# Kernel tuning notes

Measured on AMD Instinct MI355X. Metric: run time of the kernel, lower is better.

## Reference

```python
import jax, jax.numpy as jnp
import numpy as np

B, L, D = 8, 512, 1024
NUM_SPANS = 6144  # L * max_width


def setup_inputs() -> dict:
    key = jax.random.key(0)
    k_h, k_s, k_w, k_b = jax.random.split(key, 4)
    h = jax.random.normal(k_h, (B, L, D), dtype=jnp.float32)
    span_idx = jax.random.randint(k_s, (B, NUM_SPANS, 2), 0, L, dtype=jnp.int64)
    # Linear(hidden, hidden) params (xavier-ish scale)
    lim = float(np.sqrt(6.0 / (D + D)))
    W = jax.random.uniform(k_w, (D, D), dtype=jnp.float32, minval=-lim, maxval=lim)
    b = jnp.zeros((D,), dtype=jnp.float32)
    return {"h": h, "span_idx": span_idx, "W": W, "b": b}


def reference(h, span_idx, W, b):
    # h: [B, L, D]; span_idx: [B, S, 2] with S = L * width
    Bb, Ll, Dd = h.shape
    start = jnp.clip(span_idx[..., 0], 0, Ll - 1)  # [B, S]
    end = jnp.clip(span_idx[..., 1], 0, Ll - 1)    # [B, S]
    valid = start <= end                            # [B, S]
    # prefix sums: cs[i, t] = sum_{u < t} h[i, u]  -> [B, L+1, D]
    cs = jnp.concatenate([jnp.zeros((Bb, 1, Dd), h.dtype), jnp.cumsum(h, axis=1)], axis=1)
    span_sum = (jnp.take_along_axis(cs, (end + 1)[:, :, None], axis=1)
                - jnp.take_along_axis(cs, start[:, :, None], axis=1))  # [B, S, D]
    count = (end - start + 1).astype(h.dtype)[:, :, None]
    span_rep = jnp.where(valid[:, :, None], span_sum / count, 0.0)  # [B, S, D]
    out = jax.nn.relu(jnp.einsum('bsd,ed->bse', span_rep, W) + b)
    return out.reshape(Bb, Ll, -1, Dd)
```

## Files before the change

### kernel.cpp

```cpp
#include <hip/hip_runtime.h>
#include <stdint.h>

#define B_DIM 8
#define L_DIM 512
#define D_DIM 1024
#define S_DIM 6144
#define M_DIM (B_DIM * S_DIM)
#define NCHUNK 8
#define CHUNK (L_DIM / NCHUNK)

typedef __attribute__((ext_vector_type(8))) short short8;
typedef __attribute__((ext_vector_type(4))) float f32x4;
typedef __attribute__((ext_vector_type(8))) unsigned short us8;

__device__ __forceinline__ unsigned short f2bf(float f) {
    unsigned int u = __float_as_uint(f);
    u += 0x7FFFu + ((u >> 16) & 1u);
    return (unsigned short)(u >> 16);
}

__global__ __launch_bounds__(256) void chunk_sums(const float* __restrict__ h,
                                                  float* __restrict__ csum) {
    int tid = blockIdx.x * 256 + threadIdx.x;
    int d = tid & 1023;
    int c = (tid >> 10) & 7;
    int b = tid >> 13;
    const float* hp = h + ((size_t)b * L_DIM + c * CHUNK) * D_DIM + d;
    float s = 0.f;
    #pragma unroll 8
    for (int i = 0; i < CHUNK; ++i) s += hp[(size_t)i * D_DIM];
    csum[tid] = s;
}

__global__ __launch_bounds__(256) void build_cs(const float* __restrict__ h,
                                                const float* __restrict__ csum,
                                                float* __restrict__ cs) {
    int tid = blockIdx.x * 256 + threadIdx.x;
    int d = tid & 1023;
    int c = (tid >> 10) & 7;
    int b = tid >> 13;
    float p = 0.f;
    for (int cc = 0; cc < c; ++cc)
        p += csum[(b << 13) + (cc << 10) + d];
    const float* hp = h + ((size_t)b * L_DIM + c * CHUNK) * D_DIM + d;
    float* cp = cs + ((size_t)b * (L_DIM + 1) + c * CHUNK) * D_DIM + d;
    if (c == 0) cp[0] = 0.f;
    #pragma unroll 8
    for (int i = 0; i < CHUNK; ++i) {
        p += hp[(size_t)i * D_DIM];
        cp[(size_t)(i + 1) * D_DIM] = p;
    }
}

__global__ __launch_bounds__(256) void spanrep(const float* __restrict__ cs,
                                               const int* __restrict__ span_idx,
                                               unsigned short* __restrict__ rep) {
    int tid = blockIdx.x * 256 + threadIdx.x;
    int d8 = tid & 127;
    int bs = tid >> 7;
    int b = bs / S_DIM;
    int2 se = ((const int2*)span_idx)[bs];
    int st = min(max(se.x, 0), L_DIM - 1);
    int en = min(max(se.y, 0), L_DIM - 1);
    bool valid = st <= en;
    float inv = valid ? 1.0f / (float)(en - st + 1) : 0.0f;
    const float* base = cs + (size_t)b * (L_DIM + 1) * D_DIM + d8 * 8;
    const float4* pe = (const float4*)(base + (size_t)(en + 1) * D_DIM);
    const float4* ps = (const float4*)(base + (size_t)st * D_DIM);
    float4 e0 = pe[0], e1 = pe[1];
    float4 s0 = ps[0], s1 = ps[1];
    us8 o;
    o[0] = f2bf((e0.x - s0.x) * inv);
    o[1] = f2bf((e0.y - s0.y) * inv);
    o[2] = f2bf((e0.z - s0.z) * inv);
    o[3] = f2bf((e0.w - s0.w) * inv);
    o[4] = f2bf((e1.x - s1.x) * inv);
    o[5] = f2bf((e1.y - s1.y) * inv);
    o[6] = f2bf((e1.z - s1.z) * inv);
    o[7] = f2bf((e1.w - s1.w) * inv);
    *(us8*)&rep[(size_t)bs * D_DIM + d8 * 8] = o;
}

__global__ __launch_bounds__(256) void wconv(const float* __restrict__ W,
                                             unsigned short* __restrict__ Wbf) {
    int tid = blockIdx.x * 256 + threadIdx.x;
    const float4* p = (const float4*)(W + (size_t)tid * 8);
    float4 a = p[0], c = p[1];
    us8 o;
    o[0] = f2bf(a.x); o[1] = f2bf(a.y); o[2] = f2bf(a.z); o[3] = f2bf(a.w);
    o[4] = f2bf(c.x); o[5] = f2bf(c.y); o[6] = f2bf(c.z); o[7] = f2bf(c.w);
    *(us8*)&Wbf[(size_t)tid * 8] = o;
}

__global__ __launch_bounds__(256) void gemm_bias_relu(
    const unsigned short* __restrict__ A,
    const unsigned short* __restrict__ Wt,
    const float* __restrict__ bias,
    float* __restrict__ out) {
    constexpr int K = D_DIM, N = D_DIM;
    __shared__ __align__(16) unsigned short As[128 * 64];
    __shared__ __align__(16) unsigned short Bs[128 * 64];
    const int tid = threadIdx.x;
    const int wid = tid >> 6, lane = tid & 63;
    const int bn = blockIdx.x & 7;
    const int bm = blockIdx.x >> 3;
    const int wr = wid >> 1, wc = wid & 1;
    const int rowA = bm * 128;
    const int rowB = bn * 128;

    f32x4 acc[4][4];
    #pragma unroll
    for (int i = 0; i < 4; ++i)
        #pragma unroll
        for (int j = 0; j < 4; ++j) acc[i][j] = (f32x4){0.f, 0.f, 0.f, 0.f};

    for (int k0 = 0; k0 < K; k0 += 64) {
        #pragma unroll
        for (int inst = 0; inst < 4; ++inst) {
            int e = inst * 2048 + tid * 8;
            int r = e >> 6, c = e & 63;
            const unsigned short* srcA = A + (size_t)(rowA + r) * K + (k0 + c);
            const unsigned short* srcB = Wt + (size_t)(rowB + r) * K + (k0 + c);
            __builtin_amdgcn_global_load_lds(
                (const __attribute__((address_space(1))) void*)srcA,
                (__attribute__((address_space(3))) void*)&As[inst * 2048 + wid * 512],
                16, 0, 0);
            __builtin_amdgcn_global_load_lds(
                (const __attribute__((address_space(1))) void*)srcB,
                (__attribute__((address_space(3))) void*)&Bs[inst * 2048 + wid * 512],
                16, 0, 0);
        }
        asm volatile("s_waitcnt vmcnt(0)" ::: "memory");
        __syncthreads();

        #pragma unroll
        for (int ks = 0; ks < 2; ++ks) {
            const int kc = ks * 32 + (lane >> 4) * 8;
            short8 af[4], bf[4];
            #pragma unroll
            for (int i = 0; i < 4; ++i) {
                af[i] = *(const short8*)&As[(wr * 64 + i * 16 + (lane & 15)) * 64 + kc];
                bf[i] = *(const short8*)&Bs[(wc * 64 + i * 16 + (lane & 15)) * 64 + kc];
            }
            #pragma unroll
            for (int i = 0; i < 4; ++i)
                #pragma unroll
                for (int j = 0; j < 4; ++j)
                    acc[i][j] = __builtin_amdgcn_mfma_f32_16x16x32_bf16(
                        af[i], bf[j], acc[i][j], 0, 0, 0);
        }
        __syncthreads();
    }

    const int m0 = rowA + wr * 64;
    const int n0 = rowB + wc * 64;
    const int rq = lane >> 4;
    const int cl = lane & 15;
    float bv[4];
    #pragma unroll
    for (int j = 0; j < 4; ++j) bv[j] = bias[n0 + j * 16 + cl];
    #pragma unroll
    for (int i = 0; i < 4; ++i)
        #pragma unroll
        for (int j = 0; j < 4; ++j)
            #pragma unroll
            for (int r = 0; r < 4; ++r) {
                int m = m0 + i * 16 + rq * 4 + r;
                int n = n0 + j * 16 + cl;
                float v = acc[i][j][r] + bv[j];
                out[(size_t)m * N + n] = v > 0.f ? v : 0.f;
            }
}

extern "C" void kernel_launch(void* const* d_in, const int* in_sizes, int n_in,
                              void* d_out, int out_size, void* d_ws, size_t ws_size,
                              hipStream_t stream) {
    const float* h = (const float*)d_in[0];
    const int* span = (const int*)d_in[1];
    const float* W = (const float*)d_in[2];
    const float* bias = (const float*)d_in[3];
    float* out = (float*)d_out;

    char* ws = (char*)d_ws;
    float* cs = (float*)(ws);
    unsigned short* Wbf = (unsigned short*)(ws + 16809984);
    float* csum = (float*)(ws + 18907136);
    unsigned short* rep = (unsigned short*)(ws + 19169280);

    chunk_sums<<<256, 256, 0, stream>>>(h, csum);
    build_cs<<<256, 256, 0, stream>>>(h, csum, cs);
    wconv<<<512, 256, 0, stream>>>(W, Wbf);
    spanrep<<<24576, 256, 0, stream>>>(cs, span, rep);
    gemm_bias_relu<<<3072, 256, 0, stream>>>(rep, Wbf, bias, out);
}
```

Baseline: 409.1 us.

## Fuse span-mean gather into GEMM with double-buffered swizzled LDS tiles

Removes the separate spanrep kernel and its bf16 intermediate. The GEMM now gathers prefix-sum rows directly, computes span means and writes them into swizzled LDS. The GEMM moves to 512-thread blocks with 128x256 tiles, double-buffered LDS for A and B, an XOR swizzle against bank conflicts, and a block-index swizzle for L2 locality. Each N-tile re-gathers the cs rows (4x redundant reads of fp32 cs), and register pressure rises with the prefetched float4s.

```diff
diff --git a/kernel.cpp b/kernel.cpp
--- a/kernel.cpp
+++ b/kernel.cpp
@@ -1,17 +1,23 @@
 #include <hip/hip_runtime.h>
+#include <hip/hip_bf16.h>
 #include <stdint.h>
 
 #define B_DIM 8
 #define L_DIM 512
 #define D_DIM 1024
 #define S_DIM 6144
-#define M_DIM (B_DIM * S_DIM)
 #define NCHUNK 8
 #define CHUNK (L_DIM / NCHUNK)
+#define CSB (513 * 1024)
 
 typedef __attribute__((ext_vector_type(8))) short short8;
 typedef __attribute__((ext_vector_type(4))) float f32x4;
 typedef __attribute__((ext_vector_type(8))) unsigned short us8;
+
+__device__ __forceinline__ unsigned short bf16b(float x) {
+    __hip_bfloat16 h = __float2bfloat16(x);
+    return *reinterpret_cast<unsigned short*>(&h);
+}
 
 __device__ __forceinline__ unsigned short f2bf(float f) {
     unsigned int u = __float_as_uint(f);
@@ -52,35 +58,6 @@
     }
 }
 
-__global__ __launch_bounds__(256) void spanrep(const float* __restrict__ cs,
-                                               const int* __restrict__ span_idx,
-                                               unsigned short* __restrict__ rep) {
-    int tid = blockIdx.x * 256 + threadIdx.x;
-    int d8 = tid & 127;
-    int bs = tid >> 7;
-    int b = bs / S_DIM;
-    int2 se = ((const int2*)span_idx)[bs];
-    int st = min(max(se.x, 0), L_DIM - 1);
-    int en = min(max(se.y, 0), L_DIM - 1);
-    bool valid = st <= en;
-    float inv = valid ? 1.0f / (float)(en - st + 1) : 0.0f;
-    const float* base = cs + (size_t)b * (L_DIM + 1) * D_DIM + d8 * 8;
-    const float4* pe = (const float4*)(base + (size_t)(en + 1) * D_DIM);
-    const float4* ps = (const float4*)(base + (size_t)st * D_DIM);
-    float4 e0 = pe[0], e1 = pe[1];
-    float4 s0 = ps[0], s1 = ps[1];
-    us8 o;
-    o[0] = f2bf((e0.x - s0.x) * inv);
-    o[1] = f2bf((e0.y - s0.y) * inv);
-    o[2] = f2bf((e0.z - s0.z) * inv);
-    o[3] = f2bf((e0.w - s0.w) * inv);
-    o[4] = f2bf((e1.x - s1.x) * inv);
-    o[5] = f2bf((e1.y - s1.y) * inv);
-    o[6] = f2bf((e1.z - s1.z) * inv);
-    o[7] = f2bf((e1.w - s1.w) * inv);
-    *(us8*)&rep[(size_t)bs * D_DIM + d8 * 8] = o;
-}
-
 __global__ __launch_bounds__(256) void wconv(const float* __restrict__ W,
                                              unsigned short* __restrict__ Wbf) {
     int tid = blockIdx.x * 256 + threadIdx.x;
@@ -92,21 +69,57 @@
     *(us8*)&Wbf[(size_t)tid * 8] = o;
 }
 
-__global__ __launch_bounds__(256) void gemm_bias_relu(
-    const unsigned short* __restrict__ A,
-    const unsigned short* __restrict__ Wt,
+__global__ __launch_bounds__(512, 2) void fused_gemm(
+    const float* __restrict__ cs,
+    const int* __restrict__ span_idx,
+    const unsigned short* __restrict__ Wbf,
     const float* __restrict__ bias,
     float* __restrict__ out) {
     constexpr int K = D_DIM, N = D_DIM;
-    __shared__ __align__(16) unsigned short As[128 * 64];
-    __shared__ __align__(16) unsigned short Bs[128 * 64];
+    __shared__ __align__(16) unsigned short As[2][128 * 64];
+    __shared__ __align__(16) unsigned short Bs[2][256 * 64];
+    __shared__ int sOffS[128];
+    __shared__ int sOffE[128];
+    __shared__ float sInv[128];
+
     const int tid = threadIdx.x;
     const int wid = tid >> 6, lane = tid & 63;
-    const int bn = blockIdx.x & 7;
-    const int bm = blockIdx.x >> 3;
-    const int wr = wid >> 1, wc = wid & 1;
-    const int rowA = bm * 128;
-    const int rowB = bn * 128;
+    const int widbase = wid << 6;
+
+    int blk = blockIdx.x;
+    int swz = (blk & 7) * 192 + (blk >> 3);
+    const int bm = swz >> 2;
+    const int bn = swz & 3;
+    const int rowM = bm * 128;
+    const int colN = bn * 256;
+    const int b = bm / 48;
+    const float* csb = cs + (size_t)b * CSB;
+
+    if (tid < 128) {
+        int2 se = ((const int2*)span_idx)[rowM + tid];
+        int st = min(max(se.x, 0), L_DIM - 1);
+        int en = min(max(se.y, 0), L_DIM - 1);
+        float inv = (st <= en) ? 1.0f / (float)(en - st + 1) : 0.0f;
+        sOffS[tid] = st << 10;
+        sOffE[tid] = (en + 1) << 10;
+        sInv[tid] = inv;
+    }
+    __syncthreads();
+
+    const int ar0 = tid >> 3;
+    const int ac8 = tid & 7;
+    const float* pS0 = csb + sOffS[ar0] + ac8 * 8;
+    const float* pE0 = csb + sOffE[ar0] + ac8 * 8;
+    const float inv0 = sInv[ar0];
+    const float* pS1 = csb + sOffS[ar0 + 64] + ac8 * 8;
+    const float* pE1 = csb + sOffE[ar0 + 64] + ac8 * 8;
+    const float inv1 = sInv[ar0 + 64];
+    const int wa0 = ar0 * 128 + ((ac8 * 16) ^ ((ar0 & 7) << 4));
+    const int wa1 = (ar0 + 64) * 128 + ((ac8 * 16) ^ ((ar0 & 7) << 4));
+
+    const int fr = lane & 15;
+    const int kq = lane >> 4;
+    const int wr = wid >> 2, wc = wid & 3;
 
     f32x4 acc[4][4];
     #pragma unroll
@@ -114,62 +127,99 @@
         #pragma unroll
         for (int j = 0; j < 4; ++j) acc[i][j] = (f32x4){0.f, 0.f, 0.f, 0.f};
 
-    for (int k0 = 0; k0 < K; k0 += 64) {
-        #pragma unroll
-        for (int inst = 0; inst < 4; ++inst) {
-            int e = inst * 2048 + tid * 8;
-            int r = e >> 6, c = e & 63;
-            const unsigned short* srcA = A + (size_t)(rowA + r) * K + (k0 + c);
-            const unsigned short* srcB = Wt + (size_t)(rowB + r) * K + (k0 + c);
-            __builtin_amdgcn_global_load_lds(
-                (const __attribute__((address_space(1))) void*)srcA,
-                (__attribute__((address_space(3))) void*)&As[inst * 2048 + wid * 512],
-                16, 0, 0);
-            __builtin_amdgcn_global_load_lds(
-                (const __attribute__((address_space(1))) void*)srcB,
-                (__attribute__((address_space(3))) void*)&Bs[inst * 2048 + wid * 512],
-                16, 0, 0);
+    float4 eA0, eA1, sA0, sA1, eB0, eB1, sB0, sB1;
+
+#define CS_LOAD(k0v) do { \
+        eA0 = *(const float4*)(pE0 + (k0v));     eA1 = *(const float4*)(pE0 + (k0v) + 4); \
+        sA0 = *(const float4*)(pS0 + (k0v));     sA1 = *(const float4*)(pS0 + (k0v) + 4); \
+        eB0 = *(const float4*)(pE1 + (k0v));     eB1 = *(const float4*)(pE1 + (k0v) + 4); \
+        sB0 = *(const float4*)(pS1 + (k0v));     sB1 = *(const float4*)(pS1 + (k0v) + 4); \
+    } while (0)
+
+#define A_WRITE(bufi) do { \
+        us8 o0, o1; \
+        o0[0] = bf16b((eA0.x - sA0.x) * inv0); o0[1] = bf16b((eA0.y - sA0.y) * inv0); \
+        o0[2] = bf16b((eA0.z - sA0.z) * inv0); o0[3] = bf16b((eA0.w - sA0.w) * inv0); \
+        o0[4] = bf16b((eA1.x - sA1.x) * inv0); o0[5] = bf16b((eA1.y - sA1.y) * inv0); \
+        o0[6] = bf16b((eA1.z - sA1.z) * inv0); o0[7] = bf16b((eA1.w - sA1.w) * inv0); \
+        o1[0] = bf16b((eB0.x - sB0.x) * inv1); o1[1] = bf16b((eB0.y - sB0.y) * inv1); \
+        o1[2] = bf16b((eB0.z - sB0.z) * inv1); o1[3] = bf16b((eB0.w - sB0.w) * inv1); \
+        o1[4] = bf16b((eB1.x - sB1.x) * inv1); o1[5] = bf16b((eB1.y - sB1.y) * inv1); \
+        o1[6] = bf16b((eB1.z - sB1.z) * inv1); o1[7] = bf16b((eB1.w - sB1.w) * inv1); \
+        *(us8*)((char*)As[bufi] + wa0) = o0; \
+        *(us8*)((char*)As[bufi] + wa1) = o1; \
+    } while (0)
+
+#define STAGE_B(k0v, bufi) do { \
+        _Pragma("unroll") \
+        for (int i = 0; i < 4; ++i) { \
+            int ci = i * 512 + tid; \
+            int rB = ci >> 3, cB = ci & 7; \
+            const unsigned short* srcB = Wbf + (size_t)(colN + rB) * K + (k0v) + ((cB ^ (rB & 7)) * 8); \
+            __builtin_amdgcn_global_load_lds( \
+                (const __attribute__((address_space(1))) void*)srcB, \
+                (__attribute__((address_space(3))) void*)&Bs[bufi][(i * 512 + widbase) * 8], \
+                16, 0, 0); \
+        } \
+    } while (0)
+
+#define COMPUTE(bufi) do { \
+        _Pragma("unroll") \
+        for (int ks = 0; ks < 2; ++ks) { \
+            const int kb = ks * 64 + kq * 16; \
+            short8 af[4], bq[4]; \
+            _Pragma("unroll") \
+            for (int i = 0; i < 4; ++i) { \
+                int ra = wr * 64 + i * 16 + fr; \
+                af[i] = *(const short8*)((const char*)As[bufi] + ra * 128 + (kb ^ ((ra & 7) << 4))); \
+                int rb = wc * 64 + i * 16 + fr; \
+                bq[i] = *(const short8*)((const char*)Bs[bufi] + rb * 128 + (kb ^ ((rb & 7) << 4))); \
+            } \
+            _Pragma("unroll") \
+            for (int i = 0; i < 4; ++i) \
+                _Pragma("unroll") \
+                for (int j = 0; j < 4; ++j) \
+                    acc[i][j] = __builtin_amdgcn_mfma_f32_16x16x32_bf16(af[i], bq[j], acc[i][j], 0, 0, 0); \
+        } \
+    } while (0)
+
+    STAGE_B(0, 0);
+    CS_LOAD(0);
+    A_WRITE(0);
+    __syncthreads();
+
+    int buf = 0;
+    for (int t = 0; t < 16; ++t) {
+        if (t < 15) {
+            STAGE_B((t + 1) * 64, buf ^ 1);
+            CS_LOAD((t + 1) * 64);
         }
-        asm volatile("s_waitcnt vmcnt(0)" ::: "memory");
+        COMPUTE(buf);
+        if (t < 15) A_WRITE(buf ^ 1);
         __syncthreads();
-
-        #pragma unroll
-        for (int ks = 0; ks < 2; ++ks) {
-            const int kc = ks * 32 + (lane >> 4) * 8;
-            short8 af[4], bf[4];
-            #pragma unroll
-            for (int i = 0; i < 4; ++i) {
-                af[i] = *(const short8*)&As[(wr * 64 + i * 16 + (lane & 15)) * 64 + kc];
-                bf[i] = *(const short8*)&Bs[(wc * 64 + i * 16 + (lane & 15)) * 64 + kc];
-            }
-            #pragma unroll
-            for (int i = 0; i < 4; ++i)
-                #pragma unroll
-                for (int j = 0; j < 4; ++j)
-                    acc[i][j] = __builtin_amdgcn_mfma_f32_16x16x32_bf16(
-                        af[i], bf[j], acc[i][j], 0, 0, 0);
-        }
-        __syncthreads();
+        buf ^= 1;
     }
 
-    const int m0 = rowA + wr * 64;
-    const int n0 = rowB + wc * 64;
-    const int rq = lane >> 4;
-    const int cl = lane & 15;
+    const int m0 = rowM + wr * 64;
+    const int n0 = colN + wc * 64;
     float bv[4];
     #pragma unroll
-    for (int j = 0; j < 4; ++j) bv[j] = bias[n0 + j * 16 + cl];
+    for (int j = 0; j < 4; ++j) bv[j] = bias[n0 + j * 16 + fr];
     #pragma unroll
     for (int i = 0; i < 4; ++i)
         #pragma unroll
         for (int j = 0; j < 4; ++j)
             #pragma unroll
             for (int r = 0; r < 4; ++r) {
-                int m = m0 + i * 16 + rq * 4 + r;
-                int n = n0 + j * 16 + cl;
+                int m = m0 + i * 16 + kq * 4 + r;
+                int n = n0 + j * 16 + fr;
                 float v = acc[i][j][r] + bv[j];
                 out[(size_t)m * N + n] = v > 0.f ? v : 0.f;
             }
+#undef CS_LOAD
+#undef A_WRITE
+#undef STAGE_B
+#undef COMPUTE
 }
 
 extern "C" void kernel_launch(void* const* d_in, const int* in_sizes, int n_in,
@@ -185,11 +235,9 @@
     float* cs = (float*)(ws);
     unsigned short* Wbf = (unsigned short*)(ws + 16809984);
     float* csum = (float*)(ws + 18907136);
-    unsigned short* rep = (unsigned short*)(ws + 19169280);
 
     chunk_sums<<<256, 256, 0, stream>>>(h, csum);
     build_cs<<<256, 256, 0, stream>>>(h, csum, cs);
     wconv<<<512, 256, 0, stream>>>(W, Wbf);
-    spanrep<<<24576, 256, 0, stream>>>(cs, span, rep);
-    gemm_bias_relu<<<3072, 256, 0, stream>>>(rep, Wbf, bias, out);
-}
+    fused_gemm<<<1536, 512, 0, stream>>>(cs, span, Wbf, bias, out);
+}
```

Result: faster. 383.3 us (-6.3%).

## Use 256x256 double-buffered swizzled GEMM tiles and fuse prep kernels

Applied to the files above, without the earlier changes.

The GEMM moves from 128x128 tiles with 4 waves to 256x256 tiles with 8 waves and two LDS buffers, so the next K-slice loads while the current one is computed. LDS columns are XOR-swizzled to avoid bank conflicts, and the block index is remapped for L2 locality. The chunk-sum and weight-conversion kernels are merged into one launch. The larger tile needs 128KB of LDS and more accumulator registers, which lowers occupancy, and the grid shrinks to 768 blocks.

```diff
diff --git a/kernel.cpp b/kernel.cpp
--- a/kernel.cpp
+++ b/kernel.cpp
@@ -1,4 +1,5 @@
 #include <hip/hip_runtime.h>
+#include <hip/hip_bf16.h>
 #include <stdint.h>
 
 #define B_DIM 8
@@ -8,6 +9,7 @@
 #define M_DIM (B_DIM * S_DIM)
 #define NCHUNK 8
 #define CHUNK (L_DIM / NCHUNK)
+#define CSB (513 * 1024)
 
 typedef __attribute__((ext_vector_type(8))) short short8;
 typedef __attribute__((ext_vector_type(4))) float f32x4;
@@ -19,17 +21,29 @@
     return (unsigned short)(u >> 16);
 }
 
-__global__ __launch_bounds__(256) void chunk_sums(const float* __restrict__ h,
-                                                  float* __restrict__ csum) {
-    int tid = blockIdx.x * 256 + threadIdx.x;
-    int d = tid & 1023;
-    int c = (tid >> 10) & 7;
-    int b = tid >> 13;
-    const float* hp = h + ((size_t)b * L_DIM + c * CHUNK) * D_DIM + d;
-    float s = 0.f;
-    #pragma unroll 8
-    for (int i = 0; i < CHUNK; ++i) s += hp[(size_t)i * D_DIM];
-    csum[tid] = s;
+__global__ __launch_bounds__(256) void prep_fused(const float* __restrict__ h,
+                                                  float* __restrict__ csum,
+                                                  const float* __restrict__ W,
+                                                  unsigned short* __restrict__ Wbf) {
+    if (blockIdx.x < 256) {
+        int tid = blockIdx.x * 256 + threadIdx.x;
+        int d = tid & 1023;
+        int c = (tid >> 10) & 7;
+        int b = tid >> 13;
+        const float* hp = h + ((size_t)b * L_DIM + c * CHUNK) * D_DIM + d;
+        float s = 0.f;
+        #pragma unroll 8
+        for (int i = 0; i < CHUNK; ++i) s += hp[(size_t)i * D_DIM];
+        csum[tid] = s;
+    } else {
+        int tid = (blockIdx.x - 256) * 256 + threadIdx.x;
+        const float4* p = (const float4*)(W + (size_t)tid * 8);
+        float4 a = p[0], c = p[1];
+        us8 o;
+        o[0] = f2bf(a.x); o[1] = f2bf(a.y); o[2] = f2bf(a.z); o[3] = f2bf(a.w);
+        o[4] = f2bf(c.x); o[5] = f2bf(c.y); o[6] = f2bf(c.z); o[7] = f2bf(c.w);
+        *(us8*)&Wbf[(size_t)tid * 8] = o;
+    }
 }
 
 __global__ __launch_bounds__(256) void build_cs(const float* __restrict__ h,
@@ -64,7 +78,7 @@
     int en = min(max(se.y, 0), L_DIM - 1);
     bool valid = st <= en;
     float inv = valid ? 1.0f / (float)(en - st + 1) : 0.0f;
-    const float* base = cs + (size_t)b * (L_DIM + 1) * D_DIM + d8 * 8;
+    const float* base = cs + (size_t)b * CSB + d8 * 8;
     const float4* pe = (const float4*)(base + (size_t)(en + 1) * D_DIM);
     const float4* ps = (const float4*)(base + (size_t)st * D_DIM);
     float4 e0 = pe[0], e1 = pe[1];
@@ -81,95 +95,123 @@
     *(us8*)&rep[(size_t)bs * D_DIM + d8 * 8] = o;
 }
 
-__global__ __launch_bounds__(256) void wconv(const float* __restrict__ W,
-                                             unsigned short* __restrict__ Wbf) {
-    int tid = blockIdx.x * 256 + threadIdx.x;
-    const float4* p = (const float4*)(W + (size_t)tid * 8);
-    float4 a = p[0], c = p[1];
-    us8 o;
-    o[0] = f2bf(a.x); o[1] = f2bf(a.y); o[2] = f2bf(a.z); o[3] = f2bf(a.w);
-    o[4] = f2bf(c.x); o[5] = f2bf(c.y); o[6] = f2bf(c.z); o[7] = f2bf(c.w);
-    *(us8*)&Wbf[(size_t)tid * 8] = o;
-}
-
-__global__ __launch_bounds__(256) void gemm_bias_relu(
+__global__ __launch_bounds__(512, 2) void gemm_bias_relu(
     const unsigned short* __restrict__ A,
     const unsigned short* __restrict__ Wt,
     const float* __restrict__ bias,
     float* __restrict__ out) {
     constexpr int K = D_DIM, N = D_DIM;
-    __shared__ __align__(16) unsigned short As[128 * 64];
-    __shared__ __align__(16) unsigned short Bs[128 * 64];
+    __shared__ __align__(16) unsigned short As[2][256 * 64];
+    __shared__ __align__(16) unsigned short Bs[2][256 * 64];
+
     const int tid = threadIdx.x;
     const int wid = tid >> 6, lane = tid & 63;
-    const int bn = blockIdx.x & 7;
-    const int bm = blockIdx.x >> 3;
-    const int wr = wid >> 1, wc = wid & 1;
-    const int rowA = bm * 128;
-    const int rowB = bn * 128;
-
-    f32x4 acc[4][4];
+
+    int blk = blockIdx.x;
+    int swz = (blk & 7) * 96 + (blk >> 3);
+    const int bm = swz >> 2;
+    const int bn = swz & 3;
+    const int rowM = bm * 256;
+    const int colN = bn * 256;
+
+    const int fr = lane & 15;
+    const int kq = lane >> 4;
+    const int wr = wid >> 2, wc = wid & 3;
+
+    f32x4 acc[8][4];
     #pragma unroll
-    for (int i = 0; i < 4; ++i)
+    for (int i = 0; i < 8; ++i)
         #pragma unroll
         for (int j = 0; j < 4; ++j) acc[i][j] = (f32x4){0.f, 0.f, 0.f, 0.f};
 
-    for (int k0 = 0; k0 < K; k0 += 64) {
-        #pragma unroll
-        for (int inst = 0; inst < 4; ++inst) {
-            int e = inst * 2048 + tid * 8;
-            int r = e >> 6, c = e & 63;
-            const unsigned short* srcA = A + (size_t)(rowA + r) * K + (k0 + c);
-            const unsigned short* srcB = Wt + (size_t)(rowB + r) * K + (k0 + c);
-            __builtin_amdgcn_global_load_lds(
-                (const __attribute__((address_space(1))) void*)srcA,
-                (__attribute__((address_space(3))) void*)&As[inst * 2048 + wid * 512],
-                16, 0, 0);
-            __builtin_amdgcn_global_load_lds(
-                (const __attribute__((address_space(1))) void*)srcB,
-                (__attribute__((address_space(3))) void*)&Bs[inst * 2048 + wid * 512],
-                16, 0, 0);
+#define FENCE() do { asm volatile("" ::: "memory"); \
+                     __builtin_amdgcn_sched_barrier(0); } while (0)
+
+#define STAGE(k0v, bufi) do { \
+        _Pragma("unroll") \
+        for (int i = 0; i < 4; ++i) { \
+            int ci = i * 512 + tid; \
+            int r = ci >> 3, c = ci & 7; \
+            int gc = (k0v) + ((c ^ (r & 7)) * 8); \
+            const unsigned short* sa = A + (size_t)(rowM + r) * K + gc; \
+            __builtin_amdgcn_global_load_lds( \
+                (const __attribute__((address_space(1))) void*)sa, \
+                (__attribute__((address_space(3))) void*)&As[bufi][(size_t)ci * 8], \
+                16, 0, 0); \
+            const unsigned short* sb = Wt + (size_t)(colN + r) * K + gc; \
+            __builtin_amdgcn_global_load_lds( \
+                (const __attribute__((address_space(1))) void*)sb, \
+                (__attribute__((address_space(3))) void*)&Bs[bufi][(size_t)ci * 8], \
+                16, 0, 0); \
+        } \
+    } while (0)
+
+#define COMPUTE(bufi) do { \
+        _Pragma("unroll") \
+        for (int ks = 0; ks < 2; ++ks) { \
+            const int kb = ks * 64 + kq * 16; \
+            short8 af[8], bq[4]; \
+            _Pragma("unroll") \
+            for (int i = 0; i < 8; ++i) { \
+                int ra = wr * 128 + i * 16 + fr; \
+                af[i] = *(const short8*)((const char*)As[bufi] + ra * 128 + (kb ^ ((ra & 7) << 4))); \
+            } \
+            _Pragma("unroll") \
+            for (int j = 0; j < 4; ++j) { \
+                int rb = wc * 64 + j * 16 + fr; \
+                bq[j] = *(const short8*)((const char*)Bs[bufi] + rb * 128 + (kb ^ ((rb & 7) << 4))); \
+            } \
+            __builtin_amdgcn_s_setprio(1); \
+            _Pragma("unroll") \
+            for (int i = 0; i < 8; ++i) \
+                _Pragma("unroll") \
+                for (int j = 0; j < 4; ++j) \
+                    acc[i][j] = __builtin_amdgcn_mfma_f32_16x16x32_bf16(af[i], bq[j], acc[i][j], 0, 0, 0); \
+            __builtin_amdgcn_s_setprio(0); \
+        } \
+    } while (0)
+
+    STAGE(0, 0);
+    FENCE();
+    asm volatile("s_waitcnt vmcnt(0) lgkmcnt(0)" ::: "memory");
+    __builtin_amdgcn_s_barrier();
+    FENCE();
+    STAGE(64, 1);
+    FENCE();
+
+    for (int t = 0; t < 16; ++t) {
+        COMPUTE(t & 1);
+        if (t < 15) {
+            FENCE();
+            asm volatile("s_waitcnt vmcnt(0) lgkmcnt(0)" ::: "memory");
+            __builtin_amdgcn_s_barrier();
+            FENCE();
+            if (t < 14) {
+                STAGE((t + 2) * 64, t & 1);
+                FENCE();
+            }
         }
-        asm volatile("s_waitcnt vmcnt(0)" ::: "memory");
-        __syncthreads();
-
-        #pragma unroll
-        for (int ks = 0; ks < 2; ++ks) {
-            const int kc = ks * 32 + (lane >> 4) * 8;
-            short8 af[4], bf[4];
-            #pragma unroll
-            for (int i = 0; i < 4; ++i) {
-                af[i] = *(const short8*)&As[(wr * 64 + i * 16 + (lane & 15)) * 64 + kc];
-                bf[i] = *(const short8*)&Bs[(wc * 64 + i * 16 + (lane & 15)) * 64 + kc];
-            }
-            #pragma unroll
-            for (int i = 0; i < 4; ++i)
-                #pragma unroll
-                for (int j = 0; j < 4; ++j)
-                    acc[i][j] = __builtin_amdgcn_mfma_f32_16x16x32_bf16(
-                        af[i], bf[j], acc[i][j], 0, 0, 0);
-        }
-        __syncthreads();
     }
 
-    const int m0 = rowA + wr * 64;
-    const int n0 = rowB + wc * 64;
-    const int rq = lane >> 4;
-    const int cl = lane & 15;
+    const int m0 = rowM + wr * 128;
+    const int n0 = colN + wc * 64;
     float bv[4];
     #pragma unroll
-    for (int j = 0; j < 4; ++j) bv[j] = bias[n0 + j * 16 + cl];
+    for (int j = 0; j < 4; ++j) bv[j] = bias[n0 + j * 16 + fr];
     #pragma unroll
-    for (int i = 0; i < 4; ++i)
+    for (int i = 0; i < 8; ++i)
         #pragma unroll
         for (int j = 0; j < 4; ++j)
             #pragma unroll
             for (int r = 0; r < 4; ++r) {
-                int m = m0 + i * 16 + rq * 4 + r;
-                int n = n0 + j * 16 + cl;
+                int m = m0 + i * 16 + kq * 4 + r;
+                int n = n0 + j * 16 + fr;
                 float v = acc[i][j][r] + bv[j];
                 out[(size_t)m * N + n] = v > 0.f ? v : 0.f;
             }
+#undef FENCE
+#undef STAGE
+#undef COMPUTE
 }
 
 extern "C" void kernel_launch(void* const* d_in, const int* in_sizes, int n_in,
@@ -187,9 +229,8 @@
     float* csum = (float*)(ws + 18907136);
     unsigned short* rep = (unsigned short*)(ws + 19169280);
 
-    chunk_sums<<<256, 256, 0, stream>>>(h, csum);
+    prep_fused<<<768, 256, 0, stream>>>(h, csum, W, Wbf);
     build_cs<<<256, 256, 0, stream>>>(h, csum, cs);
-    wconv<<<512, 256, 0, stream>>>(W, Wbf);
     spanrep<<<24576, 256, 0, stream>>>(cs, span, rep);
-    gemm_bias_relu<<<3072, 256, 0, stream>>>(rep, Wbf, bias, out);
-}
+    gemm_bias_relu<<<768, 512, 0, stream>>>(rep, Wbf, bias, out);
+}
```

Result: faster. 379.6 us (-7.2%).
